# Kernel tuning notes

Hardware: AMD Instinct MI355X
Metric: run time of the kernel (lower is better)

The kernel has to match this reference:

```python
import jax, jax.numpy as jnp
import numpy as np

B, T, I, H, O = 512, 1024, 80, 160, 1


def setup_inputs() -> dict:
    key = jax.random.key(0)
    ks = jax.random.split(key, 11)
    s = 1.0 / np.sqrt(H)  # pytorch default init scale
    return {
        "x": jax.random.normal(ks[0], (B, T, I), dtype=jnp.float32),
        "W_ih0": jax.random.normal(ks[1], (4 * H, I), dtype=jnp.float32) * s,
        "W_hh0": jax.random.normal(ks[2], (4 * H, H), dtype=jnp.float32) * s,
        "b_ih0": jax.random.normal(ks[3], (4 * H,), dtype=jnp.float32) * s,
        "b_hh0": jax.random.normal(ks[4], (4 * H,), dtype=jnp.float32) * s,
        "W_ih1": jax.random.normal(ks[5], (4 * H, H), dtype=jnp.float32) * s,
        "W_hh1": jax.random.normal(ks[6], (4 * H, H), dtype=jnp.float32) * s,
        "b_ih1": jax.random.normal(ks[7], (4 * H,), dtype=jnp.float32) * s,
        "b_hh1": jax.random.normal(ks[8], (4 * H,), dtype=jnp.float32) * s,
        "W_out": jax.random.normal(ks[9], (O, H), dtype=jnp.float32) * s,
        "b_out": jax.random.normal(ks[10], (O,), dtype=jnp.float32) * s,
    }


def _lstm_cell(xt, h, c, W_ih, W_hh, b_ih, b_hh):
    # gates: [B, 4H], pytorch order i, f, g, o
    gates = xt @ W_ih.T + b_ih + h @ W_hh.T + b_hh
    i, f, g, o = jnp.split(gates, 4, axis=-1)
    c_new = jax.nn.sigmoid(f) * c + jax.nn.sigmoid(i) * jnp.tanh(g)
    h_new = jax.nn.sigmoid(o) * jnp.tanh(c_new)
    return h_new, c_new


def reference(x, W_ih0, W_hh0, b_ih0, b_hh0, W_ih1, W_hh1, b_ih1, b_hh1, W_out, b_out):
    Bx = x.shape[0]
    h0 = jnp.zeros((Bx, H), x.dtype)
    init = (h0, h0, h0, h0)  # (h_l0, c_l0, h_l1, c_l1)

    def step(carry, xt):
        h0_, c0_, h1_, c1_ = carry
        h0n, c0n = _lstm_cell(xt, h0_, c0_, W_ih0, W_hh0, b_ih0, b_hh0)
        h1n, c1n = _lstm_cell(h0n, h1_, c1_, W_ih1, W_hh1, b_ih1, b_hh1)
        y = jax.nn.relu(h1n @ W_out.T + b_out)  # [B, O]
        return (h0n, c0n, h1n, c1n), y

    xs = jnp.swapaxes(x, 0, 1)  # [T, B, I]
    _, ys = jax.lax.scan(step, init, xs)  # [T, B, O]
    return jnp.swapaxes(ys, 0, 1)  # [B, T, O]
```

## Files before the change

### kernel.cpp

```cpp
#include <hip/hip_runtime.h>
#include <stdint.h>


#define TT 1024
#define BATCH 512
#define II 80
#define HH 160

constexpr int BB    = 16;
constexpr int NGRP  = BATCH / BB;
constexpr int NW    = 8;
constexpr int NTHR  = NW * 64;
constexpr int NTILE = 5;
constexpr int DEPTH = 32;
constexpr int HP    = 168;
constexpr int XP    = 88;

typedef __attribute__((ext_vector_type(8))) short s8b;
typedef __attribute__((ext_vector_type(4))) short s4b;
typedef __attribute__((ext_vector_type(4))) float f4;

constexpr int SLOT_U64 = 960;
constexpr size_t OFF_RING = 4096;
constexpr size_t RING_STRIDE = (size_t)DEPTH * SLOT_U64 * 8;

constexpr int HSH_OFF = 81920;
constexpr int H0L_OFF = 92672;
constexpr int YP_OFF  = 103424;
constexpr int BS_OFF  = 104448;
constexpr int SMEM_SZ = 107648;

__device__ __forceinline__ short f2bf(float x){
  uint32_t u = __builtin_bit_cast(uint32_t, x);
  u = (u + 0x7FFFu + ((u >> 16) & 1u)) >> 16;
  return (short)u;
}
__device__ __forceinline__ float rcpf(float x){
  float r;
  asm("v_rcp_f32 %0, %1" : "=v"(r) : "v"(x));
  return r;
}
__device__ __forceinline__ float sigf(float x){ return rcpf(1.f + __expf(-x)); }
__device__ __forceinline__ float tanh_(float x){ return 1.f - 2.f*rcpf(__expf(2.f*x)+1.f); }

__device__ __forceinline__ f4 mfma16(s8b a, s8b b, f4 c){
  return __builtin_amdgcn_mfma_f32_16x16x32_bf16(a, b, c, 0, 0, 0);
}

__device__ __forceinline__ s8b pack8(float4 a, float4 b){
  s8b r;
  r[0]=f2bf(a.x); r[1]=f2bf(a.y); r[2]=f2bf(a.z); r[3]=f2bf(a.w);
  r[4]=f2bf(b.x); r[5]=f2bf(b.y); r[6]=f2bf(b.z); r[7]=f2bf(b.w);
  return r;
}
__device__ __forceinline__ float4 ld4(const float* p){ return *(const float4*)p; }
__device__ __forceinline__ s8b wfrag(const float* p){ return pack8(ld4(p), ld4(p+4)); }

__device__ __forceinline__ void st64(unsigned long long* p, unsigned long long v){
  __hip_atomic_store(p, v, __ATOMIC_RELAXED, __HIP_MEMORY_SCOPE_AGENT);
}
__device__ __forceinline__ unsigned long long ld64(const unsigned long long* p){
  return __hip_atomic_load(p, __ATOMIC_RELAXED, __HIP_MEMORY_SCOPE_AGENT);
}
__device__ __forceinline__ void poll_ge(int* p, int& shadow, int target, int lane){
  while (shadow < target){
    int v = 0;
    if (lane == 0) v = __hip_atomic_load(p, __ATOMIC_ACQUIRE, __HIP_MEMORY_SCOPE_AGENT);
    shadow = __shfl(v, 0, 64);
    if (shadow < target) __builtin_amdgcn_s_sleep(2);
  }
}

__global__ __launch_bounds__(NTHR, 1)
void lstm2(const float* __restrict__ x,
           const float* __restrict__ Wih0, const float* __restrict__ Whh0,
           const float* __restrict__ bih0, const float* __restrict__ bhh0,
           const float* __restrict__ Wih1, const float* __restrict__ Whh1,
           const float* __restrict__ bih1, const float* __restrict__ bhh1,
           const float* __restrict__ Wout, const float* __restrict__ bout,
           float* __restrict__ out, char* __restrict__ ws)
{
  extern __shared__ char smem[];
  const int tid = threadIdx.x;
  const int w   = tid >> 6;
  const int l   = tid & 63;
  const int lq  = l >> 4;
  const int lr  = l & 15;
  const int q   = l & 3;
  const int h2  = (l >> 2) & 3;
  const int stage = blockIdx.x >> 5;
  const int gid   = blockIdx.x & 31;
  const int b0    = gid * BB;
  const int li    = w*64 + l;

  int* prog = (int*)ws + gid;
  unsigned long long* ring =
      (unsigned long long*)(ws + OFF_RING + (size_t)gid * RING_STRIDE);

  short* hsh = (short*)(smem + HSH_OFF);
  const s8b zf = {};

  if (stage == 0){
    short* xsh = (short*)(smem + H0L_OFF);
    s8b Wh[NTILE][5], Wi2[NTILE];
    f4 biasv[NTILE];
    #pragma unroll
    for (int s = 0; s < NTILE; ++s){
      const int ct = w + 8*s;
      const int wrow = q*HH + 4*ct + h2;
      const int u = 4*ct + lq;
      #pragma unroll
      for (int g = 0; g < 4; ++g)
        biasv[s][g] = bih0[g*HH + u] + bhh0[g*HH + u];
      #pragma unroll
      for (int kt = 0; kt < 2; ++kt)
        *(s8b*)(smem + ((w*10 + s*2 + kt) << 10) + (l << 4)) =
            wfrag(Wih0 + (size_t)wrow*II + kt*32 + lq*8);
      Wi2[s] = (lq < 2) ? wfrag(Wih0 + (size_t)wrow*II + 64 + lq*8) : zf;
      #pragma unroll
      for (int kt = 0; kt < 5; ++kt)
        Wh[s][kt] = wfrag(Whh0 + (size_t)wrow*HH + kt*32 + lq*8);
    }
    if (w == 7){
      const float* xp = x + (size_t)(b0 + lr) * TT * II + (l>>4)*20;
      short* xd = xsh + lr*XP + (l>>4)*20;
      #pragma unroll
      for (int i = 0; i < 5; ++i){
        float4 a = ld4(xp + i*4);
        s4b p; p[0]=f2bf(a.x); p[1]=f2bf(a.y); p[2]=f2bf(a.z); p[3]=f2bf(a.w);
        *(s4b*)(xd + i*4) = p;
      }
    }
    __syncthreads();

    s8b h0a[5];
    #pragma unroll
    for (int kt = 0; kt < 5; ++kt) h0a[kt] = zf;
    float c0[NTILE] = {0.f,0.f,0.f,0.f,0.f};

    s8b xa[3];
    {
      const short* xr = xsh + lr*XP;
      xa[0] = *(const s8b*)&xr[lq*8];
      xa[1] = *(const s8b*)&xr[32 + lq*8];
      xa[2] = (lq < 2) ? *(const s8b*)&xr[64 + lq*8] : zf;
    }
    f4 accx[NTILE];
    #pragma unroll
    for (int s = 0; s < NTILE; ++s){
      accx[s] = biasv[s];
      accx[s] = mfma16(*(const s8b*)(smem + ((w*10 + s*2 + 0) << 10) + (l << 4)), xa[0], accx[s]);
      accx[s] = mfma16(*(const s8b*)(smem + ((w*10 + s*2 + 1) << 10) + (l << 4)), xa[1], accx[s]);
      accx[s] = mfma16(Wi2[s], xa[2], accx[s]);
    }

    int credB = 0;
    for (int t = 0; t < TT; ++t){
      float4 xl0, xl1, xl2, xl3, xl4;
      if (w == 7 && t+1 < TT){
        const float* xp = x + (size_t)(b0 + lr) * TT * II + (size_t)(t+1)*II + (l>>4)*20;
        xl0 = ld4(xp); xl1 = ld4(xp+4); xl2 = ld4(xp+8); xl3 = ld4(xp+12); xl4 = ld4(xp+16);
      }

      if (t >= DEPTH && credB < t - DEPTH + 1)
        poll_ge(prog, credB, t - DEPTH + 1, l);

      short* hb = hsh + (t&1)*16*HP;
      #pragma unroll
      for (int kt = 0; kt < 5; ++kt)
        #pragma unroll
        for (int s = 0; s < NTILE; ++s)
          accx[s] = mfma16(Wh[s][kt], h0a[kt], accx[s]);
      #pragma unroll
      for (int s = 0; s < NTILE; ++s){
        const float cn = sigf(accx[s][1])*c0[s] + sigf(accx[s][0])*tanh_(accx[s][2]);
        c0[s] = cn;
        const float h = sigf(accx[s][3])*tanh_(cn);
        hb[lr*HP + 4*(w + 8*s) + lq] = f2bf(h);
      }
      if (w == 7 && t+1 < TT){
        short* xd = xsh + ((t+1)&1)*16*XP + lr*XP + (l>>4)*20;
        float4 a[5] = {xl0, xl1, xl2, xl3, xl4};
        #pragma unroll
        for (int i = 0; i < 5; ++i){
          s4b p; p[0]=f2bf(a[i].x); p[1]=f2bf(a[i].y); p[2]=f2bf(a[i].z); p[3]=f2bf(a[i].w);
          *(s4b*)(xd + i*4) = p;
        }
      }
      __syncthreads();
      #pragma unroll
      for (int kt = 0; kt < 5; ++kt)
        h0a[kt] = *(const s8b*)&hb[lr*HP + kt*32 + lq*8];
      if (w < 5){
        const s8b hf = h0a[w];
        const unsigned long long tg = (unsigned long long)t;
        unsigned long long u0 = (unsigned long long)(unsigned short)hf[0]
                              | ((unsigned long long)(unsigned short)hf[1] << 16)
                              | ((unsigned long long)(unsigned short)hf[2] << 32)
                              | (tg << 48);
        unsigned long long u1 = (unsigned long long)(unsigned short)hf[3]
                              | ((unsigned long long)(unsigned short)hf[4] << 16)
                              | ((unsigned long long)(unsigned short)hf[5] << 32)
                              | (tg << 48);
        unsigned long long u2 = (unsigned long long)(unsigned short)hf[6]
                              | ((unsigned long long)(unsigned short)hf[7] << 16)
                              | (tg << 32) | (tg << 48);
        unsigned long long* sl = ring + (size_t)(t & (DEPTH-1))*SLOT_U64;
        st64(sl + li, u0); st64(sl + 320 + li, u1); st64(sl + 640 + li, u2);
      }
      {
        const short* xr = xsh + ((t+1)&1)*16*XP + lr*XP;
        xa[0] = *(const s8b*)&xr[lq*8];
        xa[1] = *(const s8b*)&xr[32 + lq*8];
        xa[2] = (lq < 2) ? *(const s8b*)&xr[64 + lq*8] : zf;
      }
      #pragma unroll
      for (int s = 0; s < NTILE; ++s){
        accx[s] = biasv[s];
        accx[s] = mfma16(*(const s8b*)(smem + ((w*10 + s*2 + 0) << 10) + (l << 4)), xa[0], accx[s]);
        accx[s] = mfma16(*(const s8b*)(smem + ((w*10 + s*2 + 1) << 10) + (l << 4)), xa[1], accx[s]);
        accx[s] = mfma16(Wi2[s], xa[2], accx[s]);
      }
    }
  }
  else {
    short* h0l = (short*)(smem + H0L_OFF);
    float* ypart = (float*)(smem + YP_OFF);
    f4* bias4 = (f4*)(smem + BS_OFF);
    for (int i = tid; i < HH; i += NTHR){
      f4 b;
      #pragma unroll
      for (int g = 0; g < 4; ++g) b[g] = bih1[g*HH + i] + bhh1[g*HH + i];
      bias4[i] = b;
    }
    s8b Wi[NTILE][3], Wh[NTILE][5];
    float woutv[NTILE];
    #pragma unroll
    for (int s = 0; s < NTILE; ++s){
      const int ct = w + 8*s;
      const int wrow = q*HH + 4*ct + h2;
      woutv[s] = Wout[4*ct + lq];
      #pragma unroll
      for (int kt = 0; kt < 5; ++kt)
        Wh[s][kt] = wfrag(Whh1 + (size_t)wrow*HH + kt*32 + lq*8);
      #pragma unroll
      for (int kt = 0; kt < 3; ++kt)
        Wi[s][kt] = wfrag(Wih1 + (size_t)wrow*HH + kt*32 + lq*8);
      #pragma unroll
      for (int kt = 3; kt < 5; ++kt)
        *(s8b*)(smem + ((w*10 + s*2 + (kt-3)) << 10) + (l << 4)) =
            wfrag(Wih1 + (size_t)wrow*HH + kt*32 + lq*8);
    }
    const float bo = bout[0];
    s8b h1a[5];
    #pragma unroll
    for (int kt = 0; kt < 5; ++kt) h1a[kt] = zf;
    float c1[NTILE] = {0.f,0.f,0.f,0.f,0.f};

    unsigned long long in0 = 0, in1 = 0, in2 = 0;
    if (w < 5){
      const unsigned long long* src = ring;
      in0 = ld64(src + li); in1 = ld64(src + 320 + li); in2 = ld64(src + 640 + li);
      bool ok = ((int)(in0>>48)==0) && ((int)(in1>>48)==0) && ((int)(in2>>48)==0);
      while (__ballot(ok) != ~0ull){
        __builtin_amdgcn_s_sleep(1);
        in0 = ld64(src + li); in1 = ld64(src + 320 + li); in2 = ld64(src + 640 + li);
        ok = ((int)(in0>>48)==0) && ((int)(in1>>48)==0) && ((int)(in2>>48)==0);
      }
      s8b v;
      v[0]=(short)in0; v[1]=(short)(in0>>16); v[2]=(short)(in0>>32);
      v[3]=(short)in1; v[4]=(short)(in1>>16); v[5]=(short)(in1>>32);
      v[6]=(short)in2; v[7]=(short)(in2>>16);
      *(s8b*)&h0l[lr*HP + w*32 + lq*8] = v;
      const unsigned long long* p1 = ring + (size_t)(1 & (DEPTH-1))*SLOT_U64;
      in0 = ld64(p1 + li); in1 = ld64(p1 + 320 + li); in2 = ld64(p1 + 640 + li);
    }
    __syncthreads();

    f4 accx[NTILE];
    {
      const short* hp = h0l;
      #pragma unroll
      for (int s = 0; s < NTILE; ++s)
        accx[s] = bias4[4*(w + 8*s) + lq];
      #pragma unroll
      for (int kt = 0; kt < 3; ++kt){
        const s8b hf = *(const s8b*)&hp[lr*HP + kt*32 + lq*8];
        #pragma unroll
        for (int s = 0; s < NTILE; ++s) accx[s] = mfma16(Wi[s][kt], hf, accx[s]);
      }
      #pragma unroll
      for (int kt = 3; kt < 5; ++kt){
        const s8b hf = *(const s8b*)&hp[lr*HP + kt*32 + lq*8];
        #pragma unroll
        for (int s = 0; s < NTILE; ++s)
          accx[s] = mfma16(*(const s8b*)(smem + ((w*10 + s*2 + (kt-3)) << 10) + (l << 4)), hf, accx[s]);
      }
    }

    for (int t = 0; t < TT; ++t){
      short* hb = hsh + (t&1)*16*HP;
      #pragma unroll
      for (int kt = 0; kt < 5; ++kt)
        #pragma unroll
        for (int s = 0; s < NTILE; ++s)
          accx[s] = mfma16(Wh[s][kt], h1a[kt], accx[s]);

      if (w < 5 && t+1 < TT){
        const int tg = t+1;
        const unsigned long long* src = ring + (size_t)(tg & (DEPTH-1))*SLOT_U64;
        bool ok = ((int)(in0>>48)==tg) && ((int)(in1>>48)==tg) && ((int)(in2>>48)==tg);
        while (__ballot(ok) != ~0ull){
          __builtin_amdgcn_s_sleep(1);
          in0 = ld64(src + li); in1 = ld64(src + 320 + li); in2 = ld64(src + 640 + li);
          ok = ((int)(in0>>48)==tg) && ((int)(in1>>48)==tg) && ((int)(in2>>48)==tg);
        }
        s8b v;
        v[0]=(short)in0; v[1]=(short)(in0>>16); v[2]=(short)(in0>>32);
        v[3]=(short)in1; v[4]=(short)(in1>>16); v[5]=(short)(in1>>32);
        v[6]=(short)in2; v[7]=(short)(in2>>16);
        *(s8b*)&h0l[((t+1)&1)*16*HP + lr*HP + w*32 + lq*8] = v;
      }

      float ysum = 0.f;
      #pragma unroll
      for (int s = 0; s < NTILE; ++s){
        const float cn = sigf(accx[s][1])*c1[s] + sigf(accx[s][0])*tanh_(accx[s][2]);
        c1[s] = cn;
        const float h = sigf(accx[s][3])*tanh_(cn);
        hb[lr*HP + 4*(w + 8*s) + lq] = f2bf(h);
        ysum += h * woutv[s];
      }
      ysum += __shfl_xor(ysum, 16, 64);
      ysum += __shfl_xor(ysum, 32, 64);
      if (l < 16) ypart[(t&1)*128 + w*16 + l] = ysum;

      __syncthreads();
      #pragma unroll
      for (int kt = 0; kt < 5; ++kt)
        h1a[kt] = *(const s8b*)&hb[lr*HP + kt*32 + lq*8];
      if (w == 0 && l < 16){
        float s_ = bo;
        #pragma unroll
        for (int ww = 0; ww < NW; ++ww) s_ += ypart[(t&1)*128 + ww*16 + l];
        out[(size_t)(b0 + l)*TT + t] = fmaxf(s_, 0.f);
      }
      {
        const short* hp = h0l + ((t+1)&1)*16*HP;
        #pragma unroll
        for (int s = 0; s < NTILE; ++s)
          accx[s] = bias4[4*(w + 8*s) + lq];
        #pragma unroll
        for (int kt = 0; kt < 3; ++kt){
          const s8b hf = *(const s8b*)&hp[lr*HP + kt*32 + lq*8];
          #pragma unroll
          for (int s = 0; s < NTILE; ++s) accx[s] = mfma16(Wi[s][kt], hf, accx[s]);
        }
        #pragma unroll
        for (int kt = 3; kt < 5; ++kt){
          const s8b hf = *(const s8b*)&hp[lr*HP + kt*32 + lq*8];
          #pragma unroll
          for (int s = 0; s < NTILE; ++s)
            accx[s] = mfma16(*(const s8b*)(smem + ((w*10 + s*2 + (kt-3)) << 10) + (l << 4)), hf, accx[s]);
        }
      }
      if (w < 5 && t+2 < TT){
        const unsigned long long* p =
            ring + (size_t)((t+2) & (DEPTH-1))*SLOT_U64;
        in0 = ld64(p + li); in1 = ld64(p + 320 + li); in2 = ld64(p + 640 + li);
      }
      if (((t & 7) == 7) && tid == 0)
        __hip_atomic_store(prog, t+1, __ATOMIC_RELEASE, __HIP_MEMORY_SCOPE_AGENT);
    }
  }
}

extern "C" void kernel_launch(void* const* d_in, const int* in_sizes, int n_in,
                              void* d_out, int out_size, void* d_ws, size_t ws_size,
                              hipStream_t stream)
{
  (void)in_sizes; (void)n_in; (void)out_size; (void)ws_size;
  (void)hipFuncSetAttribute(reinterpret_cast<const void*>(lstm2),
                            hipFuncAttributeMaxDynamicSharedMemorySize, SMEM_SZ);
  (void)hipMemsetAsync(d_ws, 0, 4096, stream);
  lstm2<<<dim3(NGRP*2), dim3(NTHR), SMEM_SZ, stream>>>(
      (const float*)d_in[0],
      (const float*)d_in[1], (const float*)d_in[2],
      (const float*)d_in[3], (const float*)d_in[4],
      (const float*)d_in[5], (const float*)d_in[6],
      (const float*)d_in[7], (const float*)d_in[8],
      (const float*)d_in[9], (const float*)d_in[10],
      (float*)d_out, (char*)d_ws);
}
```

Measured before the change: 4.459 ms.

## Offload input projections to dedicated producer blocks via tagged global rings

```diff
diff --git a/kernel.cpp b/kernel.cpp
--- a/kernel.cpp
+++ b/kernel.cpp
@@ -12,22 +12,24 @@
 constexpr int NW    = 8;
 constexpr int NTHR  = NW * 64;
 constexpr int NTILE = 5;
-constexpr int DEPTH = 32;
+constexpr int DEPTH_H = 32;
+constexpr int DEPTH_X = 8;
 constexpr int HP    = 168;
-constexpr int XP    = 88;
 
 typedef __attribute__((ext_vector_type(8))) short s8b;
-typedef __attribute__((ext_vector_type(4))) short s4b;
 typedef __attribute__((ext_vector_type(4))) float f4;
 
-constexpr int SLOT_U64 = 960;
-constexpr size_t OFF_RING = 4096;
-constexpr size_t RING_STRIDE = (size_t)DEPTH * SLOT_U64 * 8;
+constexpr int HSLOT_U64 = 960;
+constexpr size_t OFF_H = 4096;
+constexpr size_t HRING_STRIDE = (size_t)DEPTH_H * HSLOT_U64 * 8;
+constexpr int XSLOT_U64 = 5120;
+constexpr size_t OFF_X0 = OFF_H + (size_t)NGRP * HRING_STRIDE;
+constexpr size_t XRING_STRIDE = (size_t)DEPTH_X * XSLOT_U64 * 8;
+constexpr size_t OFF_X1 = OFF_X0 + (size_t)NGRP * XRING_STRIDE;
+constexpr size_t WS_TOTAL = OFF_X1 + (size_t)NGRP * XRING_STRIDE;
 
 constexpr int HSH_OFF = 81920;
-constexpr int H0L_OFF = 92672;
 constexpr int YP_OFF  = 103424;
-constexpr int BS_OFF  = 104448;
 constexpr int SMEM_SZ = 107648;
 
 __device__ __forceinline__ short f2bf(float x){
@@ -46,7 +48,6 @@
 __device__ __forceinline__ f4 mfma16(s8b a, s8b b, f4 c){
   return __builtin_amdgcn_mfma_f32_16x16x32_bf16(a, b, c, 0, 0, 0);
 }
-
 __device__ __forceinline__ s8b pack8(float4 a, float4 b){
   s8b r;
   r[0]=f2bf(a.x); r[1]=f2bf(a.y); r[2]=f2bf(a.z); r[3]=f2bf(a.w);
@@ -69,6 +70,22 @@
     shadow = __shfl(v, 0, 64);
     if (shadow < target) __builtin_amdgcn_s_sleep(2);
   }
+}
+
+__device__ __forceinline__ int tag6(int t){ return 32 | (t & 31); }
+__device__ __forceinline__ unsigned long long tagpack(float a, float b, int tg){
+  uint32_t ua = (__builtin_bit_cast(uint32_t, a) & ~7u) | (uint32_t)(tg & 7);
+  uint32_t ub = (__builtin_bit_cast(uint32_t, b) & ~7u) | (uint32_t)((tg >> 3) & 7);
+  return (unsigned long long)ua | ((unsigned long long)ub << 32);
+}
+__device__ __forceinline__ bool tagchk(unsigned long long u, int tg){
+  return (int)((u & 7u) | (((u >> 32) & 7u) << 3)) == tg;
+}
+__device__ __forceinline__ void acc_from(unsigned long long u0, unsigned long long u1, f4& a){
+  a[0] = __builtin_bit_cast(float, (uint32_t)u0);
+  a[1] = __builtin_bit_cast(float, (uint32_t)(u0 >> 32));
+  a[2] = __builtin_bit_cast(float, (uint32_t)u1);
+  a[3] = __builtin_bit_cast(float, (uint32_t)(u1 >> 32));
 }
 
 __global__ __launch_bounds__(NTHR, 1)
@@ -93,77 +110,61 @@
   const int b0    = gid * BB;
   const int li    = w*64 + l;
 
-  int* prog = (int*)ws + gid;
-  unsigned long long* ring =
-      (unsigned long long*)(ws + OFF_RING + (size_t)gid * RING_STRIDE);
+  int* progB  = (int*)ws + gid;
+  int* progA  = (int*)ws + 32 + gid;
+  int* progC1 = (int*)ws + 64 + gid;
+  unsigned long long* hring = (unsigned long long*)(ws + OFF_H  + (size_t)gid * HRING_STRIDE);
+  unsigned long long* x0r   = (unsigned long long*)(ws + OFF_X0 + (size_t)gid * XRING_STRIDE);
+  unsigned long long* x1r   = (unsigned long long*)(ws + OFF_X1 + (size_t)gid * XRING_STRIDE);
 
   short* hsh = (short*)(smem + HSH_OFF);
   const s8b zf = {};
+  const int chnk = (w*NTILE)*128;
 
   if (stage == 0){
-    short* xsh = (short*)(smem + H0L_OFF);
-    s8b Wh[NTILE][5], Wi2[NTILE];
-    f4 biasv[NTILE];
+    s8b Wh[NTILE][5];
     #pragma unroll
     for (int s = 0; s < NTILE; ++s){
       const int ct = w + 8*s;
       const int wrow = q*HH + 4*ct + h2;
-      const int u = 4*ct + lq;
-      #pragma unroll
-      for (int g = 0; g < 4; ++g)
-        biasv[s][g] = bih0[g*HH + u] + bhh0[g*HH + u];
-      #pragma unroll
-      for (int kt = 0; kt < 2; ++kt)
-        *(s8b*)(smem + ((w*10 + s*2 + kt) << 10) + (l << 4)) =
-            wfrag(Wih0 + (size_t)wrow*II + kt*32 + lq*8);
-      Wi2[s] = (lq < 2) ? wfrag(Wih0 + (size_t)wrow*II + 64 + lq*8) : zf;
       #pragma unroll
       for (int kt = 0; kt < 5; ++kt)
         Wh[s][kt] = wfrag(Whh0 + (size_t)wrow*HH + kt*32 + lq*8);
     }
-    if (w == 7){
-      const float* xp = x + (size_t)(b0 + lr) * TT * II + (l>>4)*20;
-      short* xd = xsh + lr*XP + (l>>4)*20;
-      #pragma unroll
-      for (int i = 0; i < 5; ++i){
-        float4 a = ld4(xp + i*4);
-        s4b p; p[0]=f2bf(a.x); p[1]=f2bf(a.y); p[2]=f2bf(a.z); p[3]=f2bf(a.w);
-        *(s4b*)(xd + i*4) = p;
-      }
-    }
-    __syncthreads();
-
     s8b h0a[5];
     #pragma unroll
     for (int kt = 0; kt < 5; ++kt) h0a[kt] = zf;
     float c0[NTILE] = {0.f,0.f,0.f,0.f,0.f};
 
-    s8b xa[3];
+    f4 accx[NTILE];
+    unsigned long long pa[NTILE][2];
     {
-      const short* xr = xsh + lr*XP;
-      xa[0] = *(const s8b*)&xr[lq*8];
-      xa[1] = *(const s8b*)&xr[32 + lq*8];
-      xa[2] = (lq < 2) ? *(const s8b*)&xr[64 + lq*8] : zf;
-    }
-    f4 accx[NTILE];
-    #pragma unroll
-    for (int s = 0; s < NTILE; ++s){
-      accx[s] = biasv[s];
-      accx[s] = mfma16(*(const s8b*)(smem + ((w*10 + s*2 + 0) << 10) + (l << 4)), xa[0], accx[s]);
-      accx[s] = mfma16(*(const s8b*)(smem + ((w*10 + s*2 + 1) << 10) + (l << 4)), xa[1], accx[s]);
-      accx[s] = mfma16(Wi2[s], xa[2], accx[s]);
-    }
-
-    int credB = 0;
+      const int tg = tag6(0);
+      bool ok;
+      do {
+        ok = true;
+        #pragma unroll
+        for (int s = 0; s < NTILE; ++s){
+          pa[s][0] = ld64(x0r + chnk + s*128 + 2*l);
+          pa[s][1] = ld64(x0r + chnk + s*128 + 2*l + 1);
+          ok = ok && tagchk(pa[s][0], tg) && tagchk(pa[s][1], tg);
+        }
+        if (__ballot(ok) != ~0ull){ ok = false; __builtin_amdgcn_s_sleep(1); }
+      } while (!ok);
+      #pragma unroll
+      for (int s = 0; s < NTILE; ++s) acc_from(pa[s][0], pa[s][1], accx[s]);
+      const unsigned long long* p1 = x0r + (size_t)(1 & (DEPTH_X-1))*XSLOT_U64;
+      #pragma unroll
+      for (int s = 0; s < NTILE; ++s){
+        pa[s][0] = ld64(p1 + chnk + s*128 + 2*l);
+        pa[s][1] = ld64(p1 + chnk + s*128 + 2*l + 1);
+      }
+    }
+
+    int credC1 = 0;
     for (int t = 0; t < TT; ++t){
-      float4 xl0, xl1, xl2, xl3, xl4;
-      if (w == 7 && t+1 < TT){
-        const float* xp = x + (size_t)(b0 + lr) * TT * II + (size_t)(t+1)*II + (l>>4)*20;
-        xl0 = ld4(xp); xl1 = ld4(xp+4); xl2 = ld4(xp+8); xl3 = ld4(xp+12); xl4 = ld4(xp+16);
-      }
-
-      if (t >= DEPTH && credB < t - DEPTH + 1)
-        poll_ge(prog, credB, t - DEPTH + 1, l);
+      if (t >= DEPTH_H && credC1 < t - DEPTH_H + 1)
+        poll_ge(progC1, credC1, t - DEPTH_H + 1, l);
 
       short* hb = hsh + (t&1)*16*HP;
       #pragma unroll
@@ -178,22 +179,13 @@
         const float h = sigf(accx[s][3])*tanh_(cn);
         hb[lr*HP + 4*(w + 8*s) + lq] = f2bf(h);
       }
-      if (w == 7 && t+1 < TT){
-        short* xd = xsh + ((t+1)&1)*16*XP + lr*XP + (l>>4)*20;
-        float4 a[5] = {xl0, xl1, xl2, xl3, xl4};
-        #pragma unroll
-        for (int i = 0; i < 5; ++i){
-          s4b p; p[0]=f2bf(a[i].x); p[1]=f2bf(a[i].y); p[2]=f2bf(a[i].z); p[3]=f2bf(a[i].w);
-          *(s4b*)(xd + i*4) = p;
-        }
-      }
       __syncthreads();
       #pragma unroll
       for (int kt = 0; kt < 5; ++kt)
         h0a[kt] = *(const s8b*)&hb[lr*HP + kt*32 + lq*8];
       if (w < 5){
         const s8b hf = h0a[w];
-        const unsigned long long tg = (unsigned long long)t;
+        const unsigned long long tg = (unsigned long long)(t+1);
         unsigned long long u0 = (unsigned long long)(unsigned short)hf[0]
                               | ((unsigned long long)(unsigned short)hf[1] << 16)
                               | ((unsigned long long)(unsigned short)hf[2] << 32)
@@ -205,35 +197,44 @@
         unsigned long long u2 = (unsigned long long)(unsigned short)hf[6]
                               | ((unsigned long long)(unsigned short)hf[7] << 16)
                               | (tg << 32) | (tg << 48);
-        unsigned long long* sl = ring + (size_t)(t & (DEPTH-1))*SLOT_U64;
+        unsigned long long* sl = hring + (size_t)(t & (DEPTH_H-1))*HSLOT_U64;
         st64(sl + li, u0); st64(sl + 320 + li, u1); st64(sl + 640 + li, u2);
       }
-      {
-        const short* xr = xsh + ((t+1)&1)*16*XP + lr*XP;
-        xa[0] = *(const s8b*)&xr[lq*8];
-        xa[1] = *(const s8b*)&xr[32 + lq*8];
-        xa[2] = (lq < 2) ? *(const s8b*)&xr[64 + lq*8] : zf;
-      }
-      #pragma unroll
-      for (int s = 0; s < NTILE; ++s){
-        accx[s] = biasv[s];
-        accx[s] = mfma16(*(const s8b*)(smem + ((w*10 + s*2 + 0) << 10) + (l << 4)), xa[0], accx[s]);
-        accx[s] = mfma16(*(const s8b*)(smem + ((w*10 + s*2 + 1) << 10) + (l << 4)), xa[1], accx[s]);
-        accx[s] = mfma16(Wi2[s], xa[2], accx[s]);
-      }
+      if (t+1 < TT){
+        const int tg = tag6(t+1);
+        const unsigned long long* sp = x0r + (size_t)((t+1) & (DEPTH_X-1))*XSLOT_U64;
+        bool ok = true;
+        #pragma unroll
+        for (int s = 0; s < NTILE; ++s)
+          ok = ok && tagchk(pa[s][0], tg) && tagchk(pa[s][1], tg);
+        while (__ballot(ok) != ~0ull){
+          __builtin_amdgcn_s_sleep(1);
+          ok = true;
+          #pragma unroll
+          for (int s = 0; s < NTILE; ++s){
+            pa[s][0] = ld64(sp + chnk + s*128 + 2*l);
+            pa[s][1] = ld64(sp + chnk + s*128 + 2*l + 1);
+            ok = ok && tagchk(pa[s][0], tg) && tagchk(pa[s][1], tg);
+          }
+        }
+        #pragma unroll
+        for (int s = 0; s < NTILE; ++s) acc_from(pa[s][0], pa[s][1], accx[s]);
+        if (t+2 < TT){
+          const unsigned long long* p2 = x0r + (size_t)((t+2) & (DEPTH_X-1))*XSLOT_U64;
+          #pragma unroll
+          for (int s = 0; s < NTILE; ++s){
+            pa[s][0] = ld64(p2 + chnk + s*128 + 2*l);
+            pa[s][1] = ld64(p2 + chnk + s*128 + 2*l + 1);
+          }
+        }
+      }
+      if (((t & 1) == 1) && tid == 0)
+        __hip_atomic_store(progA, t+1, __ATOMIC_RELEASE, __HIP_MEMORY_SCOPE_AGENT);
     }
   }
-  else {
-    short* h0l = (short*)(smem + H0L_OFF);
+  else if (stage == 1){
     float* ypart = (float*)(smem + YP_OFF);
-    f4* bias4 = (f4*)(smem + BS_OFF);
-    for (int i = tid; i < HH; i += NTHR){
-      f4 b;
-      #pragma unroll
-      for (int g = 0; g < 4; ++g) b[g] = bih1[g*HH + i] + bhh1[g*HH + i];
-      bias4[i] = b;
-    }
-    s8b Wi[NTILE][3], Wh[NTILE][5];
+    s8b Wh[NTILE][5];
     float woutv[NTILE];
     #pragma unroll
     for (int s = 0; s < NTILE; ++s){
@@ -243,13 +244,6 @@
       #pragma unroll
       for (int kt = 0; kt < 5; ++kt)
         Wh[s][kt] = wfrag(Whh1 + (size_t)wrow*HH + kt*32 + lq*8);
-      #pragma unroll
-      for (int kt = 0; kt < 3; ++kt)
-        Wi[s][kt] = wfrag(Wih1 + (size_t)wrow*HH + kt*32 + lq*8);
-      #pragma unroll
-      for (int kt = 3; kt < 5; ++kt)
-        *(s8b*)(smem + ((w*10 + s*2 + (kt-3)) << 10) + (l << 4)) =
-            wfrag(Wih1 + (size_t)wrow*HH + kt*32 + lq*8);
     }
     const float bo = bout[0];
     s8b h1a[5];
@@ -257,44 +251,28 @@
     for (int kt = 0; kt < 5; ++kt) h1a[kt] = zf;
     float c1[NTILE] = {0.f,0.f,0.f,0.f,0.f};
 
-    unsigned long long in0 = 0, in1 = 0, in2 = 0;
-    if (w < 5){
-      const unsigned long long* src = ring;
-      in0 = ld64(src + li); in1 = ld64(src + 320 + li); in2 = ld64(src + 640 + li);
-      bool ok = ((int)(in0>>48)==0) && ((int)(in1>>48)==0) && ((int)(in2>>48)==0);
-      while (__ballot(ok) != ~0ull){
-        __builtin_amdgcn_s_sleep(1);
-        in0 = ld64(src + li); in1 = ld64(src + 320 + li); in2 = ld64(src + 640 + li);
-        ok = ((int)(in0>>48)==0) && ((int)(in1>>48)==0) && ((int)(in2>>48)==0);
-      }
-      s8b v;
-      v[0]=(short)in0; v[1]=(short)(in0>>16); v[2]=(short)(in0>>32);
-      v[3]=(short)in1; v[4]=(short)(in1>>16); v[5]=(short)(in1>>32);
-      v[6]=(short)in2; v[7]=(short)(in2>>16);
-      *(s8b*)&h0l[lr*HP + w*32 + lq*8] = v;
-      const unsigned long long* p1 = ring + (size_t)(1 & (DEPTH-1))*SLOT_U64;
-      in0 = ld64(p1 + li); in1 = ld64(p1 + 320 + li); in2 = ld64(p1 + 640 + li);
-    }
-    __syncthreads();
-
     f4 accx[NTILE];
+    unsigned long long pa[NTILE][2];
     {
-      const short* hp = h0l;
-      #pragma unroll
-      for (int s = 0; s < NTILE; ++s)
-        accx[s] = bias4[4*(w + 8*s) + lq];
-      #pragma unroll
-      for (int kt = 0; kt < 3; ++kt){
-        const s8b hf = *(const s8b*)&hp[lr*HP + kt*32 + lq*8];
-        #pragma unroll
-        for (int s = 0; s < NTILE; ++s) accx[s] = mfma16(Wi[s][kt], hf, accx[s]);
-      }
-      #pragma unroll
-      for (int kt = 3; kt < 5; ++kt){
-        const s8b hf = *(const s8b*)&hp[lr*HP + kt*32 + lq*8];
-        #pragma unroll
-        for (int s = 0; s < NTILE; ++s)
-          accx[s] = mfma16(*(const s8b*)(smem + ((w*10 + s*2 + (kt-3)) << 10) + (l << 4)), hf, accx[s]);
+      const int tg = tag6(0);
+      bool ok;
+      do {
+        ok = true;
+        #pragma unroll
+        for (int s = 0; s < NTILE; ++s){
+          pa[s][0] = ld64(x1r + chnk + s*128 + 2*l);
+          pa[s][1] = ld64(x1r + chnk + s*128 + 2*l + 1);
+          ok = ok && tagchk(pa[s][0], tg) && tagchk(pa[s][1], tg);
+        }
+        if (__ballot(ok) != ~0ull){ ok = false; __builtin_amdgcn_s_sleep(1); }
+      } while (!ok);
+      #pragma unroll
+      for (int s = 0; s < NTILE; ++s) acc_from(pa[s][0], pa[s][1], accx[s]);
+      const unsigned long long* p1 = x1r + (size_t)(1 & (DEPTH_X-1))*XSLOT_U64;
+      #pragma unroll
+      for (int s = 0; s < NTILE; ++s){
+        pa[s][0] = ld64(p1 + chnk + s*128 + 2*l);
+        pa[s][1] = ld64(p1 + chnk + s*128 + 2*l + 1);
       }
     }
 
@@ -305,23 +283,6 @@
         #pragma unroll
         for (int s = 0; s < NTILE; ++s)
           accx[s] = mfma16(Wh[s][kt], h1a[kt], accx[s]);
-
-      if (w < 5 && t+1 < TT){
-        const int tg = t+1;
-        const unsigned long long* src = ring + (size_t)(tg & (DEPTH-1))*SLOT_U64;
-        bool ok = ((int)(in0>>48)==tg) && ((int)(in1>>48)==tg) && ((int)(in2>>48)==tg);
-        while (__ballot(ok) != ~0ull){
-          __builtin_amdgcn_s_sleep(1);
-          in0 = ld64(src + li); in1 = ld64(src + 320 + li); in2 = ld64(src + 640 + li);
-          ok = ((int)(in0>>48)==tg) && ((int)(in1>>48)==tg) && ((int)(in2>>48)==tg);
-        }
-        s8b v;
-        v[0]=(short)in0; v[1]=(short)(in0>>16); v[2]=(short)(in0>>32);
-        v[3]=(short)in1; v[4]=(short)(in1>>16); v[5]=(short)(in1>>32);
-        v[6]=(short)in2; v[7]=(short)(in2>>16);
-        *(s8b*)&h0l[((t+1)&1)*16*HP + lr*HP + w*32 + lq*8] = v;
-      }
-
       float ysum = 0.f;
       #pragma unroll
       for (int s = 0; s < NTILE; ++s){
@@ -345,32 +306,201 @@
         for (int ww = 0; ww < NW; ++ww) s_ += ypart[(t&1)*128 + ww*16 + l];
         out[(size_t)(b0 + l)*TT + t] = fmaxf(s_, 0.f);
       }
-      {
-        const short* hp = h0l + ((t+1)&1)*16*HP;
+      if (t+1 < TT){
+        const int tg = tag6(t+1);
+        const unsigned long long* sp = x1r + (size_t)((t+1) & (DEPTH_X-1))*XSLOT_U64;
+        bool ok = true;
         #pragma unroll
         for (int s = 0; s < NTILE; ++s)
-          accx[s] = bias4[4*(w + 8*s) + lq];
-        #pragma unroll
-        for (int kt = 0; kt < 3; ++kt){
-          const s8b hf = *(const s8b*)&hp[lr*HP + kt*32 + lq*8];
+          ok = ok && tagchk(pa[s][0], tg) && tagchk(pa[s][1], tg);
+        while (__ballot(ok) != ~0ull){
+          __builtin_amdgcn_s_sleep(1);
+          ok = true;
           #pragma unroll
-          for (int s = 0; s < NTILE; ++s) accx[s] = mfma16(Wi[s][kt], hf, accx[s]);
-        }
-        #pragma unroll
-        for (int kt = 3; kt < 5; ++kt){
-          const s8b hf = *(const s8b*)&hp[lr*HP + kt*32 + lq*8];
+          for (int s = 0; s < NTILE; ++s){
+            pa[s][0] = ld64(sp + chnk + s*128 + 2*l);
+            pa[s][1] = ld64(sp + chnk + s*128 + 2*l + 1);
+            ok = ok && tagchk(pa[s][0], tg) && tagchk(pa[s][1], tg);
+          }
+        }
+        #pragma unroll
+        for (int s = 0; s < NTILE; ++s) acc_from(pa[s][0], pa[s][1], accx[s]);
+        if (t+2 < TT){
+          const unsigned long long* p2 = x1r + (size_t)((t+2) & (DEPTH_X-1))*XSLOT_U64;
           #pragma unroll
-          for (int s = 0; s < NTILE; ++s)
-            accx[s] = mfma16(*(const s8b*)(smem + ((w*10 + s*2 + (kt-3)) << 10) + (l << 4)), hf, accx[s]);
-        }
-      }
-      if (w < 5 && t+2 < TT){
-        const unsigned long long* p =
-            ring + (size_t)((t+2) & (DEPTH-1))*SLOT_U64;
-        in0 = ld64(p + li); in1 = ld64(p + 320 + li); in2 = ld64(p + 640 + li);
-      }
-      if (((t & 7) == 7) && tid == 0)
-        __hip_atomic_store(prog, t+1, __ATOMIC_RELEASE, __HIP_MEMORY_SCOPE_AGENT);
+          for (int s = 0; s < NTILE; ++s){
+            pa[s][0] = ld64(p2 + chnk + s*128 + 2*l);
+            pa[s][1] = ld64(p2 + chnk + s*128 + 2*l + 1);
+          }
+        }
+      }
+      if (((t & 1) == 1) && tid == 0)
+        __hip_atomic_store(progB, t+1, __ATOMIC_RELEASE, __HIP_MEMORY_SCOPE_AGENT);
+    }
+  }
+  else if (stage == 2){
+    s8b Wi0[NTILE][2], Wi2[NTILE];
+    f4 biasv[NTILE];
+    #pragma unroll
+    for (int s = 0; s < NTILE; ++s){
+      const int ct = w + 8*s;
+      const int wrow = q*HH + 4*ct + h2;
+      const int u = 4*ct + lq;
+      #pragma unroll
+      for (int g = 0; g < 4; ++g) biasv[s][g] = bih0[g*HH + u] + bhh0[g*HH + u];
+      #pragma unroll
+      for (int kt = 0; kt < 2; ++kt)
+        Wi0[s][kt] = wfrag(Wih0 + (size_t)wrow*II + kt*32 + lq*8);
+      Wi2[s] = (lq < 2) ? wfrag(Wih0 + (size_t)wrow*II + 64 + lq*8) : zf;
+    }
+    const float* xb = x + (size_t)(b0 + lr) * TT * II;
+    s8b xa[3];
+    {
+      float4 a0 = ld4(xb + lq*8),      a1 = ld4(xb + lq*8 + 4);
+      float4 a2 = ld4(xb + 32 + lq*8), a3 = ld4(xb + 32 + lq*8 + 4);
+      const float* x2 = (lq < 2) ? xb + 64 + lq*8 : xb;
+      float4 a4 = ld4(x2), a5 = ld4(x2 + 4);
+      xa[0] = pack8(a0,a1); xa[1] = pack8(a2,a3);
+      xa[2] = (lq < 2) ? pack8(a4,a5) : zf;
+    }
+    int credA = 0;
+    for (int t = 0; t < TT; ++t){
+      const int tn = (t+1 < TT) ? t+1 : t;
+      const float* xr = xb + (size_t)tn * II;
+      float4 n0 = ld4(xr + lq*8),      n1 = ld4(xr + lq*8 + 4);
+      float4 n2 = ld4(xr + 32 + lq*8), n3 = ld4(xr + 32 + lq*8 + 4);
+      const float* x2 = (lq < 2) ? xr + 64 + lq*8 : xr;
+      float4 n4 = ld4(x2), n5 = ld4(x2 + 4);
+
+      if (t >= DEPTH_X && credA < t - DEPTH_X + 1)
+        poll_ge(progA, credA, t - DEPTH_X + 1, l);
+
+      const int tg = tag6(t);
+      unsigned long long* sp = x0r + (size_t)(t & (DEPTH_X-1))*XSLOT_U64;
+      #pragma unroll
+      for (int s = 0; s < NTILE; ++s){
+        f4 a = biasv[s];
+        a = mfma16(Wi0[s][0], xa[0], a);
+        a = mfma16(Wi0[s][1], xa[1], a);
+        a = mfma16(Wi2[s],    xa[2], a);
+        st64(sp + chnk + s*128 + 2*l,     tagpack(a[0], a[1], tg));
+        st64(sp + chnk + s*128 + 2*l + 1, tagpack(a[2], a[3], tg));
+      }
+      xa[0] = pack8(n0,n1); xa[1] = pack8(n2,n3);
+      xa[2] = (lq < 2) ? pack8(n4,n5) : zf;
+    }
+  }
+  else {
+    volatile int* c1prog = (volatile int*)smem;
+    if (l == 0) c1prog[w] = 0;
+    s8b Wi[NTILE][5];
+    f4 biasv[NTILE];
+    #pragma unroll
+    for (int s = 0; s < NTILE; ++s){
+      const int ct = w + 8*s;
+      const int wrow = q*HH + 4*ct + h2;
+      const int u = 4*ct + lq;
+      #pragma unroll
+      for (int g = 0; g < 4; ++g) biasv[s][g] = bih1[g*HH + u] + bhh1[g*HH + u];
+      #pragma unroll
+      for (int kt = 0; kt < 5; ++kt)
+        Wi[s][kt] = wfrag(Wih1 + (size_t)wrow*HH + kt*32 + lq*8);
+    }
+    __syncthreads();
+
+    s8b h0f[5];
+    unsigned long long ph[5][3];
+    {
+      bool ok;
+      do {
+        ok = true;
+        #pragma unroll
+        for (int kt = 0; kt < 5; ++kt){
+          ph[kt][0] = ld64(hring + kt*64 + l);
+          ph[kt][1] = ld64(hring + 320 + kt*64 + l);
+          ph[kt][2] = ld64(hring + 640 + kt*64 + l);
+          ok = ok && ((int)(ph[kt][0]>>48)==1) && ((int)(ph[kt][1]>>48)==1)
+                  && ((int)(ph[kt][2]>>48)==1);
+        }
+        if (__ballot(ok) != ~0ull){ ok = false; __builtin_amdgcn_s_sleep(1); }
+      } while (!ok);
+      #pragma unroll
+      for (int kt = 0; kt < 5; ++kt){
+        s8b v;
+        v[0]=(short)ph[kt][0]; v[1]=(short)(ph[kt][0]>>16); v[2]=(short)(ph[kt][0]>>32);
+        v[3]=(short)ph[kt][1]; v[4]=(short)(ph[kt][1]>>16); v[5]=(short)(ph[kt][1]>>32);
+        v[6]=(short)ph[kt][2]; v[7]=(short)(ph[kt][2]>>16);
+        h0f[kt] = v;
+      }
+      const unsigned long long* s1 = hring + (size_t)(1 & (DEPTH_H-1))*HSLOT_U64;
+      #pragma unroll
+      for (int kt = 0; kt < 5; ++kt){
+        ph[kt][0] = ld64(s1 + kt*64 + l);
+        ph[kt][1] = ld64(s1 + 320 + kt*64 + l);
+        ph[kt][2] = ld64(s1 + 640 + kt*64 + l);
+      }
+    }
+
+    int credB = 0;
+    for (int t = 0; t < TT; ++t){
+      if (t >= DEPTH_X && credB < t - DEPTH_X + 1)
+        poll_ge(progB, credB, t - DEPTH_X + 1, l);
+
+      const int tg = tag6(t);
+      unsigned long long* sp = x1r + (size_t)(t & (DEPTH_X-1))*XSLOT_U64;
+      #pragma unroll
+      for (int s = 0; s < NTILE; ++s){
+        f4 a = biasv[s];
+        #pragma unroll
+        for (int kt = 0; kt < 5; ++kt) a = mfma16(Wi[s][kt], h0f[kt], a);
+        st64(sp + chnk + s*128 + 2*l,     tagpack(a[0], a[1], tg));
+        st64(sp + chnk + s*128 + 2*l + 1, tagpack(a[2], a[3], tg));
+      }
+      if (t+1 < TT){
+        const int htg = t+2;
+        const unsigned long long* sl = hring + (size_t)((t+1) & (DEPTH_H-1))*HSLOT_U64;
+        bool ok = true;
+        #pragma unroll
+        for (int kt = 0; kt < 5; ++kt)
+          ok = ok && ((int)(ph[kt][0]>>48)==htg) && ((int)(ph[kt][1]>>48)==htg)
+                  && ((int)(ph[kt][2]>>48)==htg);
+        while (__ballot(ok) != ~0ull){
+          __builtin_amdgcn_s_sleep(1);
+          ok = true;
+          #pragma unroll
+          for (int kt = 0; kt < 5; ++kt){
+            ph[kt][0] = ld64(sl + kt*64 + l);
+            ph[kt][1] = ld64(sl + 320 + kt*64 + l);
+            ph[kt][2] = ld64(sl + 640 + kt*64 + l);
+            ok = ok && ((int)(ph[kt][0]>>48)==htg) && ((int)(ph[kt][1]>>48)==htg)
+                    && ((int)(ph[kt][2]>>48)==htg);
+          }
+        }
+        #pragma unroll
+        for (int kt = 0; kt < 5; ++kt){
+          s8b v;
+          v[0]=(short)ph[kt][0]; v[1]=(short)(ph[kt][0]>>16); v[2]=(short)(ph[kt][0]>>32);
+          v[3]=(short)ph[kt][1]; v[4]=(short)(ph[kt][1]>>16); v[5]=(short)(ph[kt][1]>>32);
+          v[6]=(short)ph[kt][2]; v[7]=(short)(ph[kt][2]>>16);
+          h0f[kt] = v;
+        }
+        if (t+2 < TT){
+          const unsigned long long* s2 = hring + (size_t)((t+2) & (DEPTH_H-1))*HSLOT_U64;
+          #pragma unroll
+          for (int kt = 0; kt < 5; ++kt){
+            ph[kt][0] = ld64(s2 + kt*64 + l);
+            ph[kt][1] = ld64(s2 + 320 + kt*64 + l);
+            ph[kt][2] = ld64(s2 + 640 + kt*64 + l);
+          }
+        }
+      }
+      if (l == 0) c1prog[w] = t + 1;
+      if (w == 0 && l == 0 && ((t & 7) == 7)){
+        int mn = c1prog[0];
+        #pragma unroll
+        for (int j = 1; j < NW; ++j){ int v = c1prog[j]; mn = v < mn ? v : mn; }
+        __hip_atomic_store(progC1, mn, __ATOMIC_RELEASE, __HIP_MEMORY_SCOPE_AGENT);
+      }
     }
   }
 }
@@ -382,8 +512,8 @@
   (void)in_sizes; (void)n_in; (void)out_size; (void)ws_size;
   (void)hipFuncSetAttribute(reinterpret_cast<const void*>(lstm2),
                             hipFuncAttributeMaxDynamicSharedMemorySize, SMEM_SZ);
-  (void)hipMemsetAsync(d_ws, 0, 4096, stream);
-  lstm2<<<dim3(NGRP*2), dim3(NTHR), SMEM_SZ, stream>>>(
+  (void)hipMemsetAsync(d_ws, 0, WS_TOTAL, stream);
+  lstm2<<<dim3(NGRP*4), dim3(NTHR), SMEM_SZ, stream>>>(
       (const float*)d_in[0],
       (const float*)d_in[1], (const float*)d_in[2],
       (const float*)d_in[3], (const float*)d_in[4],
```

After: 5.919 ms. 1.33x slower.
